# Kernel tuning notes

Measured on AMD Instinct MI355X. Metric: run time of the kernel, lower is better.

The kernel has to match this reference:

```python
import jax, jax.numpy as jnp
import numpy as np

# --- simulation constants (from MPMSimulator.__init__ / builder calls) ---
N_STEPS, N_SUBSTEPS = 20, 30          # 20 frames x 30 substeps = 600 iterations
G = 100                               # grid cells per axis (unit domain)
DX, INV_DX = 0.01, 100.0
DT = 5e-4                             # sim_dt
E, NU = 1.0e5, 0.3
MU = E / (2.0 * (1.0 + NU))
LAM = E * NU / ((1.0 + NU) * (1.0 - 2.0 * NU))
P_VOL = 0.005 ** 3                    # particle spacing 0.005
P_MASS = P_VOL * 3000.0               # density 3000
BOUND = 3                             # sticky boundary thickness (cells)
GRAVITY = np.array([0.0, -9.8, 0.0], np.float32)
_o = np.arange(3)
OFFS = np.stack(np.meshgrid(_o, _o, _o, indexing='ij'), -1).reshape(-1, 3).astype(np.int32)  # (27,3)


def setup_inputs() -> dict:
    key = jax.random.key(0)
    k1, k2 = jax.random.split(key)
    nx, ny, nz, sp = 30, 15, 30, 0.005   # add_mpm_grid dims, jitter=True
    gx = (np.arange(nx) - nx / 2) * sp + 0.5
    gy = np.arange(ny) * sp + 0.2
    gz = (np.arange(nz) - nz / 2) * sp + 0.5
    q = np.stack(np.meshgrid(gx, gy, gz, indexing='ij'), -1).reshape(-1, 3).astype(np.float32)
    jitter = jax.random.uniform(k1, q.shape, jnp.float32, 0.0, 0.5 * sp)
    particle_q = jnp.asarray(q) + jitter
    particle_qd = jnp.zeros_like(particle_q)
    v = jax.random.uniform(k2, (1,), jnp.float32, 0.5e-3, 1.5e-3)  # grid_m_ini value
    return {"v": v, "particle_q": particle_q, "particle_qd": particle_qd}


def _simulate(v, particle_q, particle_qd):
    vscalar = v[0]
    offs = jnp.asarray(OFFS)
    offs_f = offs.astype(jnp.float32)
    grav = jnp.asarray(GRAVITY)
    I3 = jnp.eye(3, dtype=jnp.float32)

    def substep(carry, _):
        x, vel, C, F = carry
        # update deformation gradient, neo-Hookean PK1 stress
        F = jnp.einsum('nij,njk->nik', I3 + DT * C, F)
        J = jnp.linalg.det(F)
        FinvT = jnp.swapaxes(jnp.linalg.inv(F), 1, 2)
        logJ = jnp.log(jnp.maximum(J, 1e-6))
        P = MU * (F - FinvT) + LAM * logJ[:, None, None] * FinvT
        stress = (-DT * P_VOL * 4.0 * INV_DX * INV_DX) * jnp.einsum('nij,nkj->nik', P, F)
        affine = stress + P_MASS * C

        # quadratic B-spline weights over 3x3x3 stencil
        base = jnp.floor(x * INV_DX - 0.5).astype(jnp.int32)          # (N,3)
        fx = x * INV_DX - base.astype(jnp.float32)                    # (N,3)
        w = jnp.stack([0.5 * (1.5 - fx) ** 2,
                       0.75 - (fx - 1.0) ** 2,
                       0.5 * (fx - 0.5) ** 2], 0)                     # (3,N,3)
        weight = (w[offs[:, 0], :, 0] * w[offs[:, 1], :, 1] * w[offs[:, 2], :, 2]).T  # (N,27)
        dpos = (offs_f[None] - fx[:, None, :]) * DX                   # (N,27,3)

        # P2G scatter (gravity folded into momentum, as p2g takes gravity)
        mom = weight[..., None] * (P_MASS * (vel + DT * grav)[:, None, :]
                                   + jnp.einsum('nij,nkj->nki', affine, dpos))  # (N,27,3)
        node = jnp.clip(base[:, None, :] + offs[None], 0, G - 1)
        idx = (node[..., 0] * G + node[..., 1]) * G + node[..., 2]    # (N,27)
        idxf = idx.reshape(-1)
        grid_v = jnp.zeros((G * G * G, 3), jnp.float32).at[idxf].add(mom.reshape(-1, 3))
        grid_m = jnp.zeros((G * G * G,), jnp.float32).at[idxf].add((weight * P_MASS).reshape(-1))

        # grid op: grid mass is initialized to grid_m_ini = v (set_optim_variables)
        gv = grid_v / (grid_m + vscalar)[:, None]
        gv3 = gv.reshape(G, G, G, 3)
        for axis in range(3):  # sticky-ish domain boundary (set_grid_bound)
            sh = [1, 1, 1]; sh[axis] = G
            ii = jnp.arange(G).reshape(sh)
            comp = gv3[..., axis]
            comp = jnp.where((ii < BOUND) & (comp < 0), 0.0, comp)
            comp = jnp.where((ii >= G - BOUND) & (comp > 0), 0.0, comp)
            gv3 = gv3.at[..., axis].set(comp)
        gv = gv3.reshape(-1, 3)

        # G2P gather
        gathered = gv[idx]                                            # (N,27,3)
        new_v = jnp.einsum('nk,nki->ni', weight, gathered)
        new_C = (4.0 * INV_DX * INV_DX) * jnp.einsum('nk,nki,nkj->nij', weight, gathered, dpos)
        return (x + DT * new_v, new_v, new_C, F), grid_m

    substep_ck = jax.checkpoint(substep)

    def frame(carry, _):
        carry, gms = jax.lax.scan(substep_ck, carry, None, length=N_SUBSTEPS)
        # extract_grad_tensor: grid mass of last substep (incl. grid_m_ini offset)
        return carry, gms[-1].reshape(G, G, G) + vscalar

    n = particle_q.shape[0]
    carry0 = (particle_q, particle_qd,
              jnp.zeros((n, 3, 3), jnp.float32),
              jnp.tile(I3, (n, 1, 1)))
    _, grid_m_seq = jax.lax.scan(jax.checkpoint(frame), carry0, None, length=N_STEPS)
    return grid_m_seq  # (N_STEPS, G, G, G)


def reference(v, particle_q, particle_qd):
    return _simulate(v, particle_q, particle_qd)
```

## Files before the change

### kernel.cpp

```cpp
#include <hip/hip_runtime.h>
#include <hip/hip_cooperative_groups.h>

namespace cg = cooperative_groups;

static constexpr int G    = 100;
static constexpr int G3   = G * G * G;
static constexpr int NP   = 13500;
static constexpr int NSUB = 600;
static constexpr int SPF  = 30;
static constexpr int NTHR = 512;
static constexpr int NBLK = 108;
static constexpr int TCIN  = 2048;
static constexpr int TCOUT = 2048;
static constexpr int CH   = (G3 + SPF - 2) / (SPF - 1);

__device__ __forceinline__ int clampi(int v) {
    return v < 0 ? 0 : (v > G - 1 ? G - 1 : v);
}

__device__ __forceinline__ float4 cell_load(const float4* p) {
    const unsigned long long* q = reinterpret_cast<const unsigned long long*>(p);
    unsigned long long a = __hip_atomic_load(&q[0], __ATOMIC_RELAXED, __HIP_MEMORY_SCOPE_AGENT);
    unsigned long long b = __hip_atomic_load(&q[1], __ATOMIC_RELAXED, __HIP_MEMORY_SCOPE_AGENT);
    float4 r;
    r.x = __uint_as_float((unsigned)(a & 0xffffffffu));
    r.y = __uint_as_float((unsigned)(a >> 32));
    r.z = __uint_as_float((unsigned)(b & 0xffffffffu));
    r.w = __uint_as_float((unsigned)(b >> 32));
    return r;
}
__device__ __forceinline__ void cell_zero(float4* p) {
    unsigned long long* q = reinterpret_cast<unsigned long long*>(p);
    __hip_atomic_store(&q[0], 0ull, __ATOMIC_RELAXED, __HIP_MEMORY_SCOPE_AGENT);
    __hip_atomic_store(&q[1], 0ull, __ATOMIC_RELAXED, __HIP_MEMORY_SCOPE_AGENT);
}

__device__ __forceinline__ void gridbar(unsigned* __restrict__ cnt,
                                        unsigned* __restrict__ flag,
                                        unsigned gen) {
    __syncthreads();
    if (threadIdx.x == 0) {
        const unsigned old = __hip_atomic_fetch_add(cnt, 1u, __ATOMIC_RELAXED, __HIP_MEMORY_SCOPE_AGENT);
        if (old == gen * (unsigned)NBLK - 1u) {
            __hip_atomic_store(flag, gen, __ATOMIC_RELEASE, __HIP_MEMORY_SCOPE_AGENT);
        } else {
            while (__hip_atomic_load(flag, __ATOMIC_RELAXED, __HIP_MEMORY_SCOPE_AGENT) < gen) {
                __builtin_amdgcn_s_sleep(2);
            }
        }
    }
    __syncthreads();
}

__launch_bounds__(NTHR)
__global__ void mpm_sim(const float* __restrict__ vscal,
                        const float* __restrict__ q0,
                        const float* __restrict__ qd0,
                        float* __restrict__ out,
                        float* __restrict__ ws,
                        unsigned* __restrict__ barcnt,
                        unsigned* __restrict__ barflag)
{
    const float vs = vscal[0];
    float4* const g4 = reinterpret_cast<float4*>(ws);

    cg::grid_group gg = cg::this_grid();
    const int tid = blockIdx.x * NTHR + threadIdx.x;
    const int nth = NBLK * NTHR;

    const int slot = threadIdx.x >> 2;
    const int sub  = threadIdx.x & 3;
    const bool act = slot < 125;
    int pid = 0;
    if (act) {
        const int b  = blockIdx.x;
        const int bx = b / 18;
        const int by = (b / 6) % 3;
        const int bz = b % 6;
        const int lx = slot / 25;
        const int rem = slot % 25;
        const int ly = rem / 5;
        const int lz = rem % 5;
        const int ix = bx * 5 + lx;
        const int iy = by * 5 + ly;
        const int iz = bz * 5 + lz;
        pid = (ix * 15 + iy) * 30 + iz;
    }

    const float DT      = 5e-4f;
    const float INV_DX  = 100.0f;
    const float DXc     = 0.01f;
    const float MU      = (float)(1.0e5 / (2.0 * (1.0 + 0.3)));
    const float LAM     = (float)(1.0e5 * 0.3 / ((1.0 + 0.3) * (1.0 - 0.6)));
    const float P_MASS  = (float)(0.005 * 0.005 * 0.005 * 3000.0);
    const float KS      = (float)(-5.0e-4 * (0.005 * 0.005 * 0.005) * 4.0 * 100.0 * 100.0);
    const float DTG     = (float)(5.0e-4 * (-9.8));
    const float CSC     = 4.0f * INV_DX * INV_DX;

    __shared__ float4 tileIn[TCIN];
    __shared__ float  tileOut[4 * TCOUT];
    __shared__ int sred[6];

    {
        const float4 z = make_float4(0.f, 0.f, 0.f, 0.f);
        for (int i = tid; i < 3 * G3; i += nth) g4[i] = z;
        if (tid == 0) {
            __hip_atomic_store(barcnt,  0u, __ATOMIC_RELAXED, __HIP_MEMORY_SCOPE_AGENT);
            __hip_atomic_store(barflag, 0u, __ATOMIC_RELAXED, __HIP_MEMORY_SCOPE_AGENT);
        }
    }

    float px = 0.f, py = 0.f, pz = 0.f, vx = 0.f, vy = 0.f, vz = 0.f;
    float C00 = 0.f, C01 = 0.f, C02 = 0.f,
          C10 = 0.f, C11 = 0.f, C12 = 0.f,
          C20 = 0.f, C21 = 0.f, C22 = 0.f;
    float F00 = 1.f, F01 = 0.f, F02 = 0.f,
          F10 = 0.f, F11 = 1.f, F12 = 0.f,
          F20 = 0.f, F21 = 0.f, F22 = 1.f;
    if (act) {
        px = q0[3 * pid + 0]; py = q0[3 * pid + 1]; pz = q0[3 * pid + 2];
        vx = qd0[3 * pid + 0]; vy = qd0[3 * pid + 1]; vz = qd0[3 * pid + 2];
    }

    int pmn0 = 0, pmn1 = 0, pmn2 = 0, pmx0 = -1, pmx1 = -1, pmx2 = -1; bool pvalid = false;
    int zmn0 = 0, zmn1 = 0, zmn2 = 0, zmx0 = -1, zmx1 = -1, zmx2 = -1; bool zvalid = false;

    gg.sync();

    unsigned gen = 0;

    for (int p = 0; p < NSUB; ++p) {
        const int bS = p % 3;
        const int bG = (p + 2) % 3;
        const int bZ = (p + 1) % 3;
        float4*       __restrict__ gS4 = g4 + bS * G3;
        const float4* __restrict__ gG4 = g4 + bG * G3;
        float4*       __restrict__ gZ4 = g4 + bZ * G3;
        const int fc = p % SPF;
        float* const outF = (fc == SPF - 1) ? (out + (p / SPF) * G3) : nullptr;

        if (threadIdx.x == 0) {
            sred[0] = INT_MAX; sred[1] = INT_MAX; sred[2] = INT_MAX;
            sred[3] = INT_MIN; sred[4] = INT_MIN; sred[5] = INT_MIN;
        }
        if (fc < SPF - 1) {
            float* of = out + (p / SPF) * G3;
            const int beg = fc * CH;
            const int end = (beg + CH < G3) ? beg + CH : G3;
            for (int i = beg + tid; i < end; i += nth)
                __hip_atomic_store(&of[i], vs, __ATOMIC_RELAXED, __HIP_MEMORY_SCOPE_AGENT);
        }
        {
            float4* t4 = reinterpret_cast<float4*>(tileOut);
            const float4 z = make_float4(0.f, 0.f, 0.f, 0.f);
            for (int i = threadIdx.x; i < TCOUT; i += NTHR) t4[i] = z;
        }
        if (zvalid) {
            const int zD1 = zmx1 - zmn1 + 1, zD2 = zmx2 - zmn2 + 1;
            const int zvol = (zmx0 - zmn0 + 1) * zD1 * zD2;
            for (int c = threadIdx.x; c < zvol; c += NTHR) {
                const int k = c % zD2;
                const int t = c / zD2;
                const int j = t % zD1;
                const int i = t / zD1;
                cell_zero(&gZ4[((zmn0 + i) * G + (zmn1 + j)) * G + (zmn2 + k)]);
            }
        }
        const int iD1 = pvalid ? (pmx1 - pmn1 + 1) : 0;
        const int iD2 = pvalid ? (pmx2 - pmn2 + 1) : 0;
        const int inVol = pvalid ? (pmx0 - pmn0 + 1) * iD1 * iD2 : 0;
        const bool staged = pvalid && (inVol <= TCIN);
        if (staged) {
            for (int c = threadIdx.x; c < inVol; c += NTHR) {
                const int k = c % iD2;
                const int t = c / iD2;
                const int j = t % iD1;
                const int i = t / iD1;
                const int nx = pmn0 + i, ny = pmn1 + j, nz = pmn2 + k;
                const float4 gq = cell_load(&gG4[(nx * G + ny) * G + nz]);
                const float den = gq.w + vs;
                float gvx = gq.x / den;
                float gvy = gq.y / den;
                float gvz = gq.z / den;
                if (nx < 3       && gvx < 0.f) gvx = 0.f;
                if (nx >= G - 3  && gvx > 0.f) gvx = 0.f;
                if (ny < 3       && gvy < 0.f) gvy = 0.f;
                if (ny >= G - 3  && gvy > 0.f) gvy = 0.f;
                if (nz < 3       && gvz < 0.f) gvz = 0.f;
                if (nz >= G - 3  && gvz > 0.f) gvz = 0.f;
                tileIn[c] = make_float4(gvx, gvy, gvz, 0.f);
            }
        }
        __syncthreads();

        int sb0 = 0, sb1 = 0, sb2 = 0;
        float fx0 = 0.f, fx1 = 0.f, fx2 = 0.f;
        float A00 = 0.f, A01 = 0.f, A02 = 0.f,
              A10 = 0.f, A11 = 0.f, A12 = 0.f,
              A20 = 0.f, A21 = 0.f, A22 = 0.f;
        float mvx = 0.f, mvy = 0.f, mvz = 0.f;

        if (act) {
            if (p > 0) {
                const float xs0 = px * INV_DX, xs1 = py * INV_DX, xs2 = pz * INV_DX;
                const float fb0 = floorf(xs0 - 0.5f), fb1 = floorf(xs1 - 0.5f), fb2 = floorf(xs2 - 0.5f);
                const int b0 = (int)fb0, b1 = (int)fb1, b2 = (int)fb2;
                const float gx0 = xs0 - fb0, gx1 = xs1 - fb1, gx2 = xs2 - fb2;
                float wa[3], wb[3], wc[3];
                wa[0] = 0.5f * (1.5f - gx0) * (1.5f - gx0);
                wa[1] = 0.75f - (gx0 - 1.0f) * (gx0 - 1.0f);
                wa[2] = 0.5f * (gx0 - 0.5f) * (gx0 - 0.5f);
                wb[0] = 0.5f * (1.5f - gx1) * (1.5f - gx1);
                wb[1] = 0.75f - (gx1 - 1.0f) * (gx1 - 1.0f);
                wb[2] = 0.5f * (gx1 - 0.5f) * (gx1 - 0.5f);
                wc[0] = 0.5f * (1.5f - gx2) * (1.5f - gx2);
                wc[1] = 0.75f - (gx2 - 1.0f) * (gx2 - 1.0f);
                wc[2] = 0.5f * (gx2 - 0.5f) * (gx2 - 0.5f);

                float nvx = 0.f, nvy = 0.f, nvz = 0.f;
                float nc00 = 0.f, nc01 = 0.f, nc02 = 0.f,
                      nc10 = 0.f, nc11 = 0.f, nc12 = 0.f,
                      nc20 = 0.f, nc21 = 0.f, nc22 = 0.f;
                #pragma unroll
                for (int t = 0; t < 7; ++t) {
                    const int c = sub + 4 * t;
                    if (c >= 27) break;
                    const int oi = c / 9;
                    const int rem = c - 9 * oi;
                    const int oj = rem / 3;
                    const int ok = rem - 3 * oj;
                    const int nx = clampi(b0 + oi);
                    const int ny = clampi(b1 + oj);
                    const int nz = clampi(b2 + ok);
                    const float dpx = ((float)oi - gx0) * DXc;
                    const float dpy = ((float)oj - gx1) * DXc;
                    const float dpz = ((float)ok - gx2) * DXc;
                    const float w = wa[oi] * wb[oj] * wc[ok];
                    float gvx, gvy, gvz;
                    if (staged) {
                        const float4 gv4 = tileIn[((nx - pmn0) * iD1 + (ny - pmn1)) * iD2 + (nz - pmn2)];
                        gvx = gv4.x; gvy = gv4.y; gvz = gv4.z;
                    } else {
                        const float4 gq = cell_load(&gG4[(nx * G + ny) * G + nz]);
                        const float den = gq.w + vs;
                        gvx = gq.x / den;
                        gvy = gq.y / den;
                        gvz = gq.z / den;
                        if (nx < 3       && gvx < 0.f) gvx = 0.f;
                        if (nx >= G - 3  && gvx > 0.f) gvx = 0.f;
                        if (ny < 3       && gvy < 0.f) gvy = 0.f;
                        if (ny >= G - 3  && gvy > 0.f) gvy = 0.f;
                        if (nz < 3       && gvz < 0.f) gvz = 0.f;
                        if (nz >= G - 3  && gvz > 0.f) gvz = 0.f;
                    }
                    nvx += w * gvx; nvy += w * gvy; nvz += w * gvz;
                    const float wgx = w * gvx, wgy = w * gvy, wgz = w * gvz;
                    nc00 += wgx * dpx; nc01 += wgx * dpy; nc02 += wgx * dpz;
                    nc10 += wgy * dpx; nc11 += wgy * dpy; nc12 += wgy * dpz;
                    nc20 += wgz * dpx; nc21 += wgz * dpy; nc22 += wgz * dpz;
                }
                #define BFLY(v) { v += __shfl_xor(v, 1); v += __shfl_xor(v, 2); }
                BFLY(nvx) BFLY(nvy) BFLY(nvz)
                BFLY(nc00) BFLY(nc01) BFLY(nc02)
                BFLY(nc10) BFLY(nc11) BFLY(nc12)
                BFLY(nc20) BFLY(nc21) BFLY(nc22)
                #undef BFLY
                vx = nvx; vy = nvy; vz = nvz;
                C00 = CSC * nc00; C01 = CSC * nc01; C02 = CSC * nc02;
                C10 = CSC * nc10; C11 = CSC * nc11; C12 = CSC * nc12;
                C20 = CSC * nc20; C21 = CSC * nc21; C22 = CSC * nc22;
                px += DT * vx; py += DT * vy; pz += DT * vz;
            }

            {
                const float t00 = F00 + DT * (C00 * F00 + C01 * F10 + C02 * F20);
                const float t01 = F01 + DT * (C00 * F01 + C01 * F11 + C02 * F21);
                const float t02 = F02 + DT * (C00 * F02 + C01 * F12 + C02 * F22);
                const float t10 = F10 + DT * (C10 * F00 + C11 * F10 + C12 * F20);
                const float t11 = F11 + DT * (C10 * F01 + C11 * F11 + C12 * F21);
                const float t12 = F12 + DT * (C10 * F02 + C11 * F12 + C12 * F22);
                const float t20 = F20 + DT * (C20 * F00 + C21 * F10 + C22 * F20);
                const float t21 = F21 + DT * (C20 * F01 + C21 * F11 + C22 * F21);
                const float t22 = F22 + DT * (C20 * F02 + C21 * F12 + C22 * F22);
                F00 = t00; F01 = t01; F02 = t02;
                F10 = t10; F11 = t11; F12 = t12;
                F20 = t20; F21 = t21; F22 = t22;
            }

            const float c00 = F11 * F22 - F12 * F21;
            const float c01 = F12 * F20 - F10 * F22;
            const float c02 = F10 * F21 - F11 * F20;
            const float det = F00 * c00 + F01 * c01 + F02 * c02;
            const float c10 = F02 * F21 - F01 * F22;
            const float c11 = F00 * F22 - F02 * F20;
            const float c12 = F01 * F20 - F00 * F21;
            const float c20 = F01 * F12 - F02 * F11;
            const float c21 = F02 * F10 - F00 * F12;
            const float c22 = F00 * F11 - F01 * F10;
            const float idet = 1.0f / det;
            const float lj = LAM * logf(fmaxf(det, 1e-6f));
            const float fit00 = c00 * idet, fit01 = c01 * idet, fit02 = c02 * idet;
            const float fit10 = c10 * idet, fit11 = c11 * idet, fit12 = c12 * idet;
            const float fit20 = c20 * idet, fit21 = c21 * idet, fit22 = c22 * idet;
            const float P00 = MU * (F00 - fit00) + lj * fit00;
            const float P01 = MU * (F01 - fit01) + lj * fit01;
            const float P02 = MU * (F02 - fit02) + lj * fit02;
            const float P10 = MU * (F10 - fit10) + lj * fit10;
            const float P11 = MU * (F11 - fit11) + lj * fit11;
            const float P12 = MU * (F12 - fit12) + lj * fit12;
            const float P20 = MU * (F20 - fit20) + lj * fit20;
            const float P21 = MU * (F21 - fit21) + lj * fit21;
            const float P22 = MU * (F22 - fit22) + lj * fit22;
            A00 = KS * (P00 * F00 + P01 * F01 + P02 * F02) + P_MASS * C00;
            A01 = KS * (P00 * F10 + P01 * F11 + P02 * F12) + P_MASS * C01;
            A02 = KS * (P00 * F20 + P01 * F21 + P02 * F22) + P_MASS * C02;
            A10 = KS * (P10 * F00 + P11 * F01 + P12 * F02) + P_MASS * C10;
            A11 = KS * (P10 * F10 + P11 * F11 + P12 * F12) + P_MASS * C11;
            A12 = KS * (P10 * F20 + P11 * F21 + P12 * F22) + P_MASS * C12;
            A20 = KS * (P20 * F00 + P21 * F01 + P22 * F02) + P_MASS * C20;
            A21 = KS * (P20 * F10 + P21 * F11 + P22 * F12) + P_MASS * C21;
            A22 = KS * (P20 * F20 + P21 * F21 + P22 * F22) + P_MASS * C22;

            const float xs0 = px * INV_DX, xs1 = py * INV_DX, xs2 = pz * INV_DX;
            const float fb0 = floorf(xs0 - 0.5f), fb1 = floorf(xs1 - 0.5f), fb2 = floorf(xs2 - 0.5f);
            sb0 = (int)fb0; sb1 = (int)fb1; sb2 = (int)fb2;
            fx0 = xs0 - fb0; fx1 = xs1 - fb1; fx2 = xs2 - fb2;
            mvx = P_MASS * vx;
            mvy = P_MASS * (vy + DTG);
            mvz = P_MASS * vz;

            if (sub == 0) {
                atomicMin(&sred[0], clampi(sb0)); atomicMax(&sred[3], clampi(sb0 + 2));
                atomicMin(&sred[1], clampi(sb1)); atomicMax(&sred[4], clampi(sb1 + 2));
                atomicMin(&sred[2], clampi(sb2)); atomicMax(&sred[5], clampi(sb2 + 2));
            }
        }
        __syncthreads();

        const int mn0 = sred[0], mn1 = sred[1], mn2 = sred[2];
        const int mx0 = sred[3], mx1 = sred[4], mx2 = sred[5];
        const bool anyAct = (mx0 >= mn0);
        const int D1 = mx1 - mn1 + 1, D2 = mx2 - mn2 + 1;
        const int vol = anyAct ? (mx0 - mn0 + 1) * D1 * D2 : 0;
        const bool useLDS = anyAct && (vol <= TCOUT);

        float wa0 = 0.f, wa1 = 0.f, wa2 = 0.f, wb0 = 0.f, wb1 = 0.f, wb2 = 0.f,
              wcc0 = 0.f, wcc1 = 0.f, wcc2 = 0.f;
        if (act) {
            wa0 = 0.5f * (1.5f - fx0) * (1.5f - fx0);
            wa1 = 0.75f - (fx0 - 1.0f) * (fx0 - 1.0f);
            wa2 = 0.5f * (fx0 - 0.5f) * (fx0 - 0.5f);
            wb0 = 0.5f * (1.5f - fx1) * (1.5f - fx1);
            wb1 = 0.75f - (fx1 - 1.0f) * (fx1 - 1.0f);
            wb2 = 0.5f * (fx1 - 0.5f) * (fx1 - 0.5f);
            wcc0 = 0.5f * (1.5f - fx2) * (1.5f - fx2);
            wcc1 = 0.75f - (fx2 - 1.0f) * (fx2 - 1.0f);
            wcc2 = 0.5f * (fx2 - 0.5f) * (fx2 - 0.5f);
        }
        const float WA[3] = { wa0, wa1, wa2 };
        const float WB[3] = { wb0, wb1, wb2 };
        const float WC[3] = { wcc0, wcc1, wcc2 };

        if (useLDS) {
            if (act) {
                #pragma unroll
                for (int t = 0; t < 7; ++t) {
                    const int c = sub + 4 * t;
                    if (c >= 27) break;
                    const int oi = c / 9;
                    const int rem = c - 9 * oi;
                    const int oj = rem / 3;
                    const int ok = rem - 3 * oj;
                    const int li  = clampi(sb0 + oi) - mn0;
                    const int lj2 = clampi(sb1 + oj) - mn1;
                    const int lk  = clampi(sb2 + ok) - mn2;
                    const float dpx = ((float)oi - fx0) * DXc;
                    const float dpy = ((float)oj - fx1) * DXc;
                    const float dpz = ((float)ok - fx2) * DXc;
                    const float w = WA[oi] * WB[oj] * WC[ok];
                    const int c4 = 4 * ((li * D1 + lj2) * D2 + lk);
                    atomicAdd(&tileOut[c4 + 0], w * (mvx + A00 * dpx + A01 * dpy + A02 * dpz));
                    atomicAdd(&tileOut[c4 + 1], w * (mvy + A10 * dpx + A11 * dpy + A12 * dpz));
                    atomicAdd(&tileOut[c4 + 2], w * (mvz + A20 * dpx + A21 * dpy + A22 * dpz));
                    atomicAdd(&tileOut[c4 + 3], w * P_MASS);
                }
            }
            __syncthreads();
            for (int c = threadIdx.x; c < vol; c += NTHR) {
                const float m = tileOut[4 * c + 3];
                if (m != 0.f) {
                    const int k = c % D2;
                    const int t = c / D2;
                    const int j = t % D1;
                    const int i = t / D1;
                    const int gidx = ((mn0 + i) * G + (mn1 + j)) * G + (mn2 + k);
                    float* gp = reinterpret_cast<float*>(gS4 + gidx);
                    unsafeAtomicAdd(gp + 0, tileOut[4 * c + 0]);
                    unsafeAtomicAdd(gp + 1, tileOut[4 * c + 1]);
                    unsafeAtomicAdd(gp + 2, tileOut[4 * c + 2]);
                    unsafeAtomicAdd(gp + 3, m);
                    if (outF) unsafeAtomicAdd(&outF[gidx], m);
                }
            }
        } else {
            if (anyAct && act) {
                #pragma unroll
                for (int t = 0; t < 7; ++t) {
                    const int c = sub + 4 * t;
                    if (c >= 27) break;
                    const int oi = c / 9;
                    const int rem = c - 9 * oi;
                    const int oj = rem / 3;
                    const int ok = rem - 3 * oj;
                    const int nx = clampi(sb0 + oi);
                    const int ny = clampi(sb1 + oj);
                    const int nz = clampi(sb2 + ok);
                    const float dpx = ((float)oi - fx0) * DXc;
                    const float dpy = ((float)oj - fx1) * DXc;
                    const float dpz = ((float)ok - fx2) * DXc;
                    const float w = WA[oi] * WB[oj] * WC[ok];
                    const int gidx = (nx * G + ny) * G + nz;
                    float* gp = reinterpret_cast<float*>(gS4 + gidx);
                    unsafeAtomicAdd(gp + 0, w * (mvx + A00 * dpx + A01 * dpy + A02 * dpz));
                    unsafeAtomicAdd(gp + 1, w * (mvy + A10 * dpx + A11 * dpy + A12 * dpz));
                    unsafeAtomicAdd(gp + 2, w * (mvz + A20 * dpx + A21 * dpy + A22 * dpz));
                    unsafeAtomicAdd(gp + 3, w * P_MASS);
                    if (outF) unsafeAtomicAdd(&outF[gidx], w * P_MASS);
                }
            }
            __syncthreads();
        }

        zmn0 = pmn0; zmn1 = pmn1; zmn2 = pmn2;
        zmx0 = pmx0; zmx1 = pmx1; zmx2 = pmx2; zvalid = pvalid;
        pmn0 = mn0; pmn1 = mn1; pmn2 = mn2;
        pmx0 = mx0; pmx1 = mx1; pmx2 = mx2; pvalid = anyAct;

        if (p < NSUB - 1) gridbar(barcnt, barflag, ++gen);
    }
}

extern "C" void kernel_launch(void* const* d_in, const int* in_sizes, int n_in,
                              void* d_out, int out_size, void* d_ws, size_t ws_size,
                              hipStream_t stream) {
    const float* v  = (const float*)d_in[0];
    const float* q  = (const float*)d_in[1];
    const float* qd = (const float*)d_in[2];
    float* out = (float*)d_out;
    float* ws  = (float*)d_ws;
    char* tail = (char*)d_ws + (ws_size & ~(size_t)255);
    unsigned* barcnt  = reinterpret_cast<unsigned*>(tail - 256);
    unsigned* barflag = reinterpret_cast<unsigned*>(tail - 512);
    void* args[] = { (void*)&v, (void*)&q, (void*)&qd, (void*)&out, (void*)&ws,
                     (void*)&barcnt, (void*)&barflag };
    hipLaunchCooperativeKernel(reinterpret_cast<void*>(mpm_sim),
                               dim3(NBLK), dim3(NTHR), args, 0, stream);
}
```

Baseline: 17.74 ms.

## Predict P2G tile bounds from previous bbox and let all threads spin at barrier

```diff
diff --git a/kernel.cpp b/kernel.cpp
--- a/kernel.cpp
+++ b/kernel.cpp
@@ -17,6 +17,8 @@
 __device__ __forceinline__ int clampi(int v) {
     return v < 0 ? 0 : (v > G - 1 ? G - 1 : v);
 }
+__device__ __forceinline__ int maxi(int a, int b) { return a > b ? a : b; }
+__device__ __forceinline__ int mini(int a, int b) { return a < b ? a : b; }
 
 __device__ __forceinline__ float4 cell_load(const float4* p) {
     const unsigned long long* q = reinterpret_cast<const unsigned long long*>(p);
@@ -43,13 +45,10 @@
         const unsigned old = __hip_atomic_fetch_add(cnt, 1u, __ATOMIC_RELAXED, __HIP_MEMORY_SCOPE_AGENT);
         if (old == gen * (unsigned)NBLK - 1u) {
             __hip_atomic_store(flag, gen, __ATOMIC_RELEASE, __HIP_MEMORY_SCOPE_AGENT);
-        } else {
-            while (__hip_atomic_load(flag, __ATOMIC_RELAXED, __HIP_MEMORY_SCOPE_AGENT) < gen) {
-                __builtin_amdgcn_s_sleep(2);
-            }
         }
     }
-    __syncthreads();
+    while (__hip_atomic_load(flag, __ATOMIC_RELAXED, __HIP_MEMORY_SCOPE_AGENT) < gen) { }
+    asm volatile("" ::: "memory");
 }
 
 __launch_bounds__(NTHR)
@@ -139,6 +138,15 @@
         const int fc = p % SPF;
         float* const outF = (fc == SPF - 1) ? (out + (p / SPF) * G3) : nullptr;
 
+        const int tmn0 = pvalid ? maxi(pmn0 - 1, 0) : 0;
+        const int tmn1 = pvalid ? maxi(pmn1 - 1, 0) : 0;
+        const int tmn2 = pvalid ? maxi(pmn2 - 1, 0) : 0;
+        const int tD0  = pvalid ? (mini(pmx0 + 1, G - 1) - tmn0 + 1) : 0;
+        const int tD1  = pvalid ? (mini(pmx1 + 1, G - 1) - tmn1 + 1) : 0;
+        const int tD2  = pvalid ? (mini(pmx2 + 1, G - 1) - tmn2 + 1) : 0;
+        const int tvol = pvalid ? tD0 * tD1 * tD2 : 0;
+        const bool fast = pvalid && (tvol <= TCOUT);
+
         if (threadIdx.x == 0) {
             sred[0] = INT_MAX; sred[1] = INT_MAX; sred[2] = INT_MAX;
             sred[3] = INT_MIN; sred[4] = INT_MIN; sred[5] = INT_MIN;
@@ -153,7 +161,8 @@
         {
             float4* t4 = reinterpret_cast<float4*>(tileOut);
             const float4 z = make_float4(0.f, 0.f, 0.f, 0.f);
-            for (int i = threadIdx.x; i < TCOUT; i += NTHR) t4[i] = z;
+            const int zn = fast ? tvol : TCOUT;
+            for (int i = threadIdx.x; i < zn; i += NTHR) t4[i] = z;
         }
         if (zvalid) {
             const int zD1 = zmx1 - zmn1 + 1, zD2 = zmx2 - zmn2 + 1;
@@ -335,14 +344,6 @@
                 atomicMin(&sred[2], clampi(sb2)); atomicMax(&sred[5], clampi(sb2 + 2));
             }
         }
-        __syncthreads();
-
-        const int mn0 = sred[0], mn1 = sred[1], mn2 = sred[2];
-        const int mx0 = sred[3], mx1 = sred[4], mx2 = sred[5];
-        const bool anyAct = (mx0 >= mn0);
-        const int D1 = mx1 - mn1 + 1, D2 = mx2 - mn2 + 1;
-        const int vol = anyAct ? (mx0 - mn0 + 1) * D1 * D2 : 0;
-        const bool useLDS = anyAct && (vol <= TCOUT);
 
         float wa0 = 0.f, wa1 = 0.f, wa2 = 0.f, wb0 = 0.f, wb1 = 0.f, wb2 = 0.f,
               wcc0 = 0.f, wcc1 = 0.f, wcc2 = 0.f;
@@ -361,7 +362,7 @@
         const float WB[3] = { wb0, wb1, wb2 };
         const float WC[3] = { wcc0, wcc1, wcc2 };
 
-        if (useLDS) {
+        if (fast) {
             if (act) {
                 #pragma unroll
                 for (int t = 0; t < 7; ++t) {
@@ -371,14 +372,14 @@
                     const int rem = c - 9 * oi;
                     const int oj = rem / 3;
                     const int ok = rem - 3 * oj;
-                    const int li  = clampi(sb0 + oi) - mn0;
-                    const int lj2 = clampi(sb1 + oj) - mn1;
-                    const int lk  = clampi(sb2 + ok) - mn2;
+                    const int li  = clampi(sb0 + oi) - tmn0;
+                    const int lj2 = clampi(sb1 + oj) - tmn1;
+                    const int lk  = clampi(sb2 + ok) - tmn2;
                     const float dpx = ((float)oi - fx0) * DXc;
                     const float dpy = ((float)oj - fx1) * DXc;
                     const float dpz = ((float)ok - fx2) * DXc;
                     const float w = WA[oi] * WB[oj] * WC[ok];
-                    const int c4 = 4 * ((li * D1 + lj2) * D2 + lk);
+                    const int c4 = 4 * ((li * tD1 + lj2) * tD2 + lk);
                     atomicAdd(&tileOut[c4 + 0], w * (mvx + A00 * dpx + A01 * dpy + A02 * dpz));
                     atomicAdd(&tileOut[c4 + 1], w * (mvy + A10 * dpx + A11 * dpy + A12 * dpz));
                     atomicAdd(&tileOut[c4 + 2], w * (mvz + A20 * dpx + A21 * dpy + A22 * dpz));
@@ -386,14 +387,14 @@
                 }
             }
             __syncthreads();
-            for (int c = threadIdx.x; c < vol; c += NTHR) {
+            for (int c = threadIdx.x; c < tvol; c += NTHR) {
                 const float m = tileOut[4 * c + 3];
                 if (m != 0.f) {
-                    const int k = c % D2;
-                    const int t = c / D2;
-                    const int j = t % D1;
-                    const int i = t / D1;
-                    const int gidx = ((mn0 + i) * G + (mn1 + j)) * G + (mn2 + k);
+                    const int k = c % tD2;
+                    const int t = c / tD2;
+                    const int j = t % tD1;
+                    const int i = t / tD1;
+                    const int gidx = ((tmn0 + i) * G + (tmn1 + j)) * G + (tmn2 + k);
                     float* gp = reinterpret_cast<float*>(gS4 + gidx);
                     unsafeAtomicAdd(gp + 0, tileOut[4 * c + 0]);
                     unsafeAtomicAdd(gp + 1, tileOut[4 * c + 1]);
@@ -403,38 +404,88 @@
                 }
             }
         } else {
-            if (anyAct && act) {
-                #pragma unroll
-                for (int t = 0; t < 7; ++t) {
-                    const int c = sub + 4 * t;
-                    if (c >= 27) break;
-                    const int oi = c / 9;
-                    const int rem = c - 9 * oi;
-                    const int oj = rem / 3;
-                    const int ok = rem - 3 * oj;
-                    const int nx = clampi(sb0 + oi);
-                    const int ny = clampi(sb1 + oj);
-                    const int nz = clampi(sb2 + ok);
-                    const float dpx = ((float)oi - fx0) * DXc;
-                    const float dpy = ((float)oj - fx1) * DXc;
-                    const float dpz = ((float)ok - fx2) * DXc;
-                    const float w = WA[oi] * WB[oj] * WC[ok];
-                    const int gidx = (nx * G + ny) * G + nz;
-                    float* gp = reinterpret_cast<float*>(gS4 + gidx);
-                    unsafeAtomicAdd(gp + 0, w * (mvx + A00 * dpx + A01 * dpy + A02 * dpz));
-                    unsafeAtomicAdd(gp + 1, w * (mvy + A10 * dpx + A11 * dpy + A12 * dpz));
-                    unsafeAtomicAdd(gp + 2, w * (mvz + A20 * dpx + A21 * dpy + A22 * dpz));
-                    unsafeAtomicAdd(gp + 3, w * P_MASS);
-                    if (outF) unsafeAtomicAdd(&outF[gidx], w * P_MASS);
+            __syncthreads();
+            const int mn0 = sred[0], mn1 = sred[1], mn2 = sred[2];
+            const int mx0 = sred[3], mx1 = sred[4], mx2 = sred[5];
+            const bool anyAct = (mx0 >= mn0);
+            const int D1 = mx1 - mn1 + 1, D2 = mx2 - mn2 + 1;
+            const int vol = anyAct ? (mx0 - mn0 + 1) * D1 * D2 : 0;
+            const bool useLDS = anyAct && (vol <= TCOUT);
+            if (useLDS) {
+                if (act) {
+                    #pragma unroll
+                    for (int t = 0; t < 7; ++t) {
+                        const int c = sub + 4 * t;
+                        if (c >= 27) break;
+                        const int oi = c / 9;
+                        const int rem = c - 9 * oi;
+                        const int oj = rem / 3;
+                        const int ok = rem - 3 * oj;
+                        const int li  = clampi(sb0 + oi) - mn0;
+                        const int lj2 = clampi(sb1 + oj) - mn1;
+                        const int lk  = clampi(sb2 + ok) - mn2;
+                        const float dpx = ((float)oi - fx0) * DXc;
+                        const float dpy = ((float)oj - fx1) * DXc;
+                        const float dpz = ((float)ok - fx2) * DXc;
+                        const float w = WA[oi] * WB[oj] * WC[ok];
+                        const int c4 = 4 * ((li * D1 + lj2) * D2 + lk);
+                        atomicAdd(&tileOut[c4 + 0], w * (mvx + A00 * dpx + A01 * dpy + A02 * dpz));
+                        atomicAdd(&tileOut[c4 + 1], w * (mvy + A10 * dpx + A11 * dpy + A12 * dpz));
+                        atomicAdd(&tileOut[c4 + 2], w * (mvz + A20 * dpx + A21 * dpy + A22 * dpz));
+                        atomicAdd(&tileOut[c4 + 3], w * P_MASS);
+                    }
                 }
-            }
-            __syncthreads();
+                __syncthreads();
+                for (int c = threadIdx.x; c < vol; c += NTHR) {
+                    const float m = tileOut[4 * c + 3];
+                    if (m != 0.f) {
+                        const int k = c % D2;
+                        const int t = c / D2;
+                        const int j = t % D1;
+                        const int i = t / D1;
+                        const int gidx = ((mn0 + i) * G + (mn1 + j)) * G + (mn2 + k);
+                        float* gp = reinterpret_cast<float*>(gS4 + gidx);
+                        unsafeAtomicAdd(gp + 0, tileOut[4 * c + 0]);
+                        unsafeAtomicAdd(gp + 1, tileOut[4 * c + 1]);
+                        unsafeAtomicAdd(gp + 2, tileOut[4 * c + 2]);
+                        unsafeAtomicAdd(gp + 3, m);
+                        if (outF) unsafeAtomicAdd(&outF[gidx], m);
+                    }
+                }
+            } else {
+                if (anyAct && act) {
+                    #pragma unroll
+                    for (int t = 0; t < 7; ++t) {
+                        const int c = sub + 4 * t;
+                        if (c >= 27) break;
+                        const int oi = c / 9;
+                        const int rem = c - 9 * oi;
+                        const int oj = rem / 3;
+                        const int ok = rem - 3 * oj;
+                        const int nx = clampi(sb0 + oi);
+                        const int ny = clampi(sb1 + oj);
+                        const int nz = clampi(sb2 + ok);
+                        const float dpx = ((float)oi - fx0) * DXc;
+                        const float dpy = ((float)oj - fx1) * DXc;
+                        const float dpz = ((float)ok - fx2) * DXc;
+                        const float w = WA[oi] * WB[oj] * WC[ok];
+                        const int gidx = (nx * G + ny) * G + nz;
+                        float* gp = reinterpret_cast<float*>(gS4 + gidx);
+                        unsafeAtomicAdd(gp + 0, w * (mvx + A00 * dpx + A01 * dpy + A02 * dpz));
+                        unsafeAtomicAdd(gp + 1, w * (mvy + A10 * dpx + A11 * dpy + A12 * dpz));
+                        unsafeAtomicAdd(gp + 2, w * (mvz + A20 * dpx + A21 * dpy + A22 * dpz));
+                        unsafeAtomicAdd(gp + 3, w * P_MASS);
+                        if (outF) unsafeAtomicAdd(&outF[gidx], w * P_MASS);
+                    }
+                }
+                __syncthreads();
+            }
         }
 
         zmn0 = pmn0; zmn1 = pmn1; zmn2 = pmn2;
         zmx0 = pmx0; zmx1 = pmx1; zmx2 = pmx2; zvalid = pvalid;
-        pmn0 = mn0; pmn1 = mn1; pmn2 = mn2;
-        pmx0 = mx0; pmx1 = mx1; pmx2 = mx2; pvalid = anyAct;
+        pmn0 = sred[0]; pmn1 = sred[1]; pmn2 = sred[2];
+        pmx0 = sred[3]; pmx1 = sred[4]; pmx2 = sred[5]; pvalid = (pmx0 >= pmn0);
 
         if (p < NSUB - 1) gridbar(barcnt, barflag, ++gen);
     }
```

Measured after the change: 17.39 ms. -2.0%, faster.
